# Kernel optimization log

Hardware: AMD Instinct MI355X
Metric: run time of the kernel (lower is better)

## Reference

```python
import jax, jax.numpy as jnp
import numpy as np

B, C, Ci, V = 1024, 256, 128, 90
EPS = 1e-5


def setup_inputs() -> dict:
    key = jax.random.key(0)
    ks = iter(jax.random.split(key, 40))
    def nrm(shape, s=1.0):
        return jax.random.normal(next(ks), shape, jnp.float32) * s
    def uni(shape):
        return jax.random.uniform(next(ks), shape, jnp.float32, 0.5, 1.5)
    inp = {"x1": nrm((B, C, V)), "x2": nrm((B, C, V))}
    for p in ["g", "th", "ph"]:
        inp[p + "_bn_gamma"] = uni((C,))
        inp[p + "_bn_beta"] = nrm((C,), 0.1)
        inp[p + "_bn_mean"] = nrm((C,), 0.1)
        inp[p + "_bn_var"] = uni((C,))
        inp[p + "_w"] = nrm((Ci, C), 0.05)
        inp[p + "_b"] = nrm((Ci,), 0.05)
    inp["W_w"] = nrm((C, Ci), 0.05)
    inp["W_b"] = nrm((C,), 0.05)
    inp["W_bn_gamma"] = uni((C,))
    inp["W_bn_beta"] = nrm((C,), 0.1)
    inp["W_bn_mean"] = nrm((C,), 0.1)
    inp["W_bn_var"] = uni((C,))
    inp["qt_w"] = nrm((Ci, C), 0.05); inp["qt_b"] = nrm((Ci,), 0.05)
    inp["ks_w"] = nrm((Ci, V), 0.05); inp["ks_b"] = nrm((Ci,), 0.05)
    inp["qs_w"] = nrm((Ci, V), 0.05); inp["qs_b"] = nrm((Ci,), 0.05)
    inp["kt_w"] = nrm((Ci, C), 0.05); inp["kt_b"] = nrm((Ci,), 0.05)
    return inp


def _bn(x, g, b, m, v):
    # eval-mode BatchNorm1d over channel dim of (B, C, V)
    return (x - m[:, None]) * jax.lax.rsqrt(v[:, None] + EPS) * g[:, None] + b[:, None]


def _conv1(x, w, b):
    # 1x1 Conv1d: (B, Cin, V) x (Cout, Cin) -> (B, Cout, V)
    return jnp.einsum('bcv,oc->bov', x, w) + b[:, None]


def reference(x1, x2,
              g_bn_gamma, g_bn_beta, g_bn_mean, g_bn_var, g_w, g_b,
              th_bn_gamma, th_bn_beta, th_bn_mean, th_bn_var, th_w, th_b,
              ph_bn_gamma, ph_bn_beta, ph_bn_mean, ph_bn_var, ph_w, ph_b,
              W_w, W_b, W_bn_gamma, W_bn_beta, W_bn_mean, W_bn_var,
              qt_w, qt_b, ks_w, ks_b, qs_w, qs_b, kt_w, kt_b):
    g_x1 = _conv1(_bn(x1, g_bn_gamma, g_bn_beta, g_bn_mean, g_bn_var), g_w, g_b)
    g_x2 = _conv1(_bn(x2, g_bn_gamma, g_bn_beta, g_bn_mean, g_bn_var), g_w, g_b)
    theta = _conv1(_bn(x1, th_bn_gamma, th_bn_beta, th_bn_mean, th_bn_var), th_w, th_b)  # theta(x1)
    phi = _conv1(_bn(x2, ph_bn_gamma, ph_bn_beta, ph_bn_mean, ph_bn_var), ph_w, ph_b)    # phi(x2)

    e_time = jnp.einsum('biv,bjv->bij', theta, phi)   # (B, Ci, Ci) = theta_x1 @ phi_x2
    e_space = jnp.einsum('bci,bcj->bij', theta, phi)  # (B, V, V)  = theta_x2 @ phi_x1

    attn_time_1 = jax.nn.softmax(e_time, axis=-1)
    attn_time_2 = jax.nn.softmax(jnp.swapaxes(e_time, 1, 2), axis=-1)
    attn_space_2 = jax.nn.softmax(e_space, axis=-1)
    attn_space_1 = jax.nn.softmax(jnp.swapaxes(e_space, 1, 2), axis=-1)

    z1 = jnp.einsum('bij,bjv,bvw->biw', attn_time_2, g_x1, attn_space_2)  # (B, Ci, V)
    z2 = jnp.einsum('bij,bjv,bvw->biw', attn_time_1, g_x2, attn_space_1)

    m1t = x1.mean(axis=2)                      # (B, C)
    q_time = m1t @ qt_w.T + qt_b               # (B, Ci)
    k_space = x2.mean(axis=1) @ ks_w.T + ks_b  # (B, Ci)
    # bmm of (B,1,Ci) x (B,Ci,1) -> (B,1,1); softmax over singleton dim == 1 (kept for faithfulness)
    attn_t2s = jax.nn.softmax(jnp.sum(q_time * k_space, axis=-1, keepdims=True)[:, :, None], axis=-1)
    x2n = x2 + attn_t2s * m1t[:, :, None]      # broadcast (B,1,1)*(B,C,1) over V

    q_space = x1.mean(axis=1) @ qs_w.T + qs_b  # (B, Ci)
    k_time = x2n.mean(axis=2) @ kt_w.T + kt_b  # (B, Ci)
    attn_s2t = jax.nn.softmax(jnp.sum(q_space * k_time, axis=-1, keepdims=True)[:, :, None], axis=-1)
    x1n = x1 + attn_s2t * x2n.mean(axis=1)[:, None, :]

    def Wop(z):
        return _bn(_conv1(z, W_w, W_b), W_bn_gamma, W_bn_beta, W_bn_mean, W_bn_var)

    return (x1n + Wop(z1), x2n + Wop(z2))
```

## Files before the change

### kernel.cpp

```cpp
#include <hip/hip_runtime.h>

namespace {

constexpr int B = 1024;

using u16 = unsigned short;
using u32 = unsigned int;

typedef __attribute__((ext_vector_type(8))) short bf16x8;
typedef __attribute__((ext_vector_type(4))) float f32x4;

#define MFMA16(a, b, c) __builtin_amdgcn_mfma_f32_16x16x32_bf16(a, b, c, 0, 0, 0)

__device__ __forceinline__ u16 f2bf(float f) {
  u32 u = __builtin_bit_cast(u32, f);
  u += 0x7FFFu + ((u >> 16) & 1u);
  return (u16)(u >> 16);
}
__device__ __forceinline__ float bf2f(u16 s) {
  u32 u = ((u32)s) << 16;
  return __builtin_bit_cast(float, u);
}
__device__ __forceinline__ u32 packbf2(float a, float b) {
  return (u32)f2bf(a) | ((u32)f2bf(b) << 16);
}

__global__ __launch_bounds__(256) void k0_fold(
    const float* __restrict__ gg, const float* __restrict__ gbe, const float* __restrict__ gme, const float* __restrict__ gva,
    const float* __restrict__ gw, const float* __restrict__ gbi,
    const float* __restrict__ tg, const float* __restrict__ tbe, const float* __restrict__ tme, const float* __restrict__ tva,
    const float* __restrict__ tw, const float* __restrict__ tbi,
    const float* __restrict__ pg, const float* __restrict__ pbe, const float* __restrict__ pme, const float* __restrict__ pva,
    const float* __restrict__ pw, const float* __restrict__ pbi,
    const float* __restrict__ Ww, const float* __restrict__ Wb,
    const float* __restrict__ Wg2, const float* __restrict__ Wbe, const float* __restrict__ Wme, const float* __restrict__ Wva,
    u16* __restrict__ wgo, float* __restrict__ bgo,
    u16* __restrict__ wthi, u16* __restrict__ wtlo, float* __restrict__ bto,
    u16* __restrict__ wphi, u16* __restrict__ wplo, float* __restrict__ bpo,
    u16* __restrict__ wWo, float* __restrict__ bWo)
{
  __shared__ float red[4];
  const int blk = blockIdx.x, tid = threadIdx.x;
  if (blk < 384) {
    const int p = blk >> 7, o = blk & 127;
    const float *ga, *be, *me, *va, *wm, *bi;
    if (p == 0)      { ga = gg; be = gbe; me = gme; va = gva; wm = gw; bi = gbi; }
    else if (p == 1) { ga = tg; be = tbe; me = tme; va = tva; wm = tw; bi = tbi; }
    else             { ga = pg; be = pbe; me = pme; va = pva; wm = pw; bi = pbi; }
    float s = ga[tid] * rsqrtf(va[tid] + 1e-5f);
    float t = be[tid] - me[tid] * s;
    float wv = wm[o * 256 + tid];
    float val = wv * s;
    if (p == 0) {
      wgo[o * 256 + tid] = f2bf(val);
    } else {
      u16 hi = f2bf(val);
      u16 lo = f2bf(val - bf2f(hi));
      if (p == 1) { wthi[o * 256 + tid] = hi; wtlo[o * 256 + tid] = lo; }
      else        { wphi[o * 256 + tid] = hi; wplo[o * 256 + tid] = lo; }
    }
    float part = t * wv;
#pragma unroll
    for (int off = 32; off; off >>= 1) part += __shfl_down(part, off);
    if ((tid & 63) == 0) red[tid >> 6] = part;
    __syncthreads();
    if (tid == 0) {
      float bsum = bi[o] + red[0] + red[1] + red[2] + red[3];
      if (p == 0) bgo[o] = bsum; else if (p == 1) bto[o] = bsum; else bpo[o] = bsum;
    }
  } else {
    const int c = blk - 384;
    float sW = Wg2[c] * rsqrtf(Wva[c] + 1e-5f);
    if (tid < 128) wWo[c * 128 + tid] = f2bf(Ww[c * 128 + tid] * sW);
    if (tid == 0) bWo[c] = Wb[c] * sW + Wbe[c] - Wme[c] * sW;
  }
}

__global__ __launch_bounds__(512, 4) void k1_conv(
    const float* __restrict__ x1, const float* __restrict__ x2,
    const u16* __restrict__ wG, const float* __restrict__ bG,
    const u16* __restrict__ wTh, const u16* __restrict__ wTl, const float* __restrict__ bT,
    const u16* __restrict__ wPh, const u16* __restrict__ wPl, const float* __restrict__ bP,
    u32* __restrict__ thRm, u32* __restrict__ phRm,
    u16* __restrict__ outU,
    float* __restrict__ m1t, float* __restrict__ x2cm, float* __restrict__ x1am)
{
  __shared__ u32 qb[64 * 92];
  __shared__ u16 xh[96 * 136];
  __shared__ u16 xl[96 * 136];
  __shared__ float red[4];
  const int b = blockIdx.x, tid = threadIdx.x;
  const int l = tid & 63, wv = tid >> 6, lr = l & 15, lq = l >> 4;
  const f32x4 zero = {0.f, 0.f, 0.f, 0.f};

  auto doPhase = [&](const float* __restrict__ xb,
                     const u16* __restrict__ Wh, const u16* __restrict__ Wl, const float* __restrict__ biasT,
                     u32* __restrict__ rmDst, u32* __restrict__ pkDst, u16* __restrict__ gDst, bool isX1) {
    f32x4 aT[6], aG[6];
#pragma unroll
    for (int i = 0; i < 6; ++i) { aT[i] = zero; aG[i] = zero; }
    float cs = 0.f;
    for (int h = 0; h < 2; ++h) {
      for (int q = 0; q < 2; ++q) {
        __syncthreads();
        const float* src = xb + (2 * h + q) * 5760;
        for (int t = tid; t < 2880; t += 512) {
          float2 f = *(const float2*)(src + 2 * t);
          int cl = (2 * t) / 90, v = 2 * t - 90 * cl;
          u16 h0 = f2bf(f.x); u16 l0 = f2bf(f.x - bf2f(h0));
          u16 h1 = f2bf(f.y); u16 l1 = f2bf(f.y - bf2f(h1));
          uint2 w; w.x = (u32)h0 | ((u32)l0 << 16); w.y = (u32)h1 | ((u32)l1 << 16);
          *(uint2*)&qb[cl * 92 + v] = w;
        }
        __syncthreads();
        for (int t = tid; t < 1440; t += 512) {
          int v = t % 90, c4 = t / 90;
          u32 p0 = qb[(4 * c4 + 0) * 92 + v], p1 = qb[(4 * c4 + 1) * 92 + v];
          u32 p2 = qb[(4 * c4 + 2) * 92 + v], p3 = qb[(4 * c4 + 3) * 92 + v];
          uint2 hi, lo;
          hi.x = (p0 & 0xFFFFu) | (p1 << 16);
          hi.y = (p2 & 0xFFFFu) | (p3 << 16);
          lo.x = (p0 >> 16) | (p1 & 0xFFFF0000u);
          lo.y = (p2 >> 16) | (p3 & 0xFFFF0000u);
          int base = v * 136 + 64 * q + 4 * c4;
          *(uint2*)&xh[base] = hi;
          *(uint2*)&xl[base] = lo;
        }
        if (q == 1) {
          for (int t = tid; t < 384; t += 512) {
            int v = 90 + (t >> 6), c2 = (t & 63) * 2;
            *(u32*)&xh[v * 136 + c2] = 0u;
            *(u32*)&xl[v * 136 + c2] = 0u;
          }
        }
      }
      __syncthreads();
      if (isX1) {
        if (tid < 128) {
          float s = 0.f;
          for (int v = 0; v < 90; ++v) s += bf2f(xh[v * 136 + tid]) + bf2f(xl[v * 136 + tid]);
          m1t[b * 256 + 128 * h + tid] = s * (1.f / 90.f);
#pragma unroll
          for (int o = 32; o; o >>= 1) s += __shfl_down(s, o);
          if ((tid & 63) == 0) red[(tid >> 6) + 2 * h] = s;
        }
      } else {
        if (tid < 90) {
          float s = 0.f;
          for (int cl = 0; cl < 128; ++cl) s += bf2f(xh[tid * 136 + cl]) + bf2f(xl[tid * 136 + cl]);
          cs += s;
        }
      }
      for (int kk = 0; kk < 4; ++kk) {
        const int wo = (16 * wv + lr) * 256 + 128 * h + kk * 32 + 8 * lq;
        bf16x8 ah = *(const bf16x8*)(Wh + wo);
        bf16x8 al = *(const bf16x8*)(Wl + wo);
        bf16x8 ag = *(const bf16x8*)(wG + wo);
#pragma unroll
        for (int nt = 0; nt < 6; ++nt) {
          const int bo = (16 * nt + lr) * 136 + kk * 32 + 8 * lq;
          bf16x8 bh = *(const bf16x8*)&xh[bo];
          bf16x8 bl = *(const bf16x8*)&xl[bo];
          aT[nt] = MFMA16(ah, bh, aT[nt]);
          aT[nt] = MFMA16(ah, bl, aT[nt]);
          aT[nt] = MFMA16(al, bh, aT[nt]);
          aG[nt] = MFMA16(ag, bh, aG[nt]);
        }
      }
    }
    __syncthreads();
    const int c0 = 16 * wv + 4 * lq;
    const float4 bt4 = *(const float4*)(biasT + c0);
    const float4 bg4 = *(const float4*)(bG + c0);
#pragma unroll
    for (int nt = 0; nt < 6; ++nt) {
      const int v = 16 * nt + lr;
      u32 pk0, pk1, pk2, pk3; uint2 gpk;
      if (v < 90) {
        float t0 = aT[nt][0] + bt4.x, t1 = aT[nt][1] + bt4.y;
        float t2 = aT[nt][2] + bt4.z, t3 = aT[nt][3] + bt4.w;
        u16 h0 = f2bf(t0), h1 = f2bf(t1), h2 = f2bf(t2), h3 = f2bf(t3);
        pk0 = (u32)h0 | ((u32)f2bf(t0 - bf2f(h0)) << 16);
        pk1 = (u32)h1 | ((u32)f2bf(t1 - bf2f(h1)) << 16);
        pk2 = (u32)h2 | ((u32)f2bf(t2 - bf2f(h2)) << 16);
        pk3 = (u32)h3 | ((u32)f2bf(t3 - bf2f(h3)) << 16);
        gpk.x = packbf2(aG[nt][0] + bg4.x, aG[nt][1] + bg4.y);
        gpk.y = packbf2(aG[nt][2] + bg4.z, aG[nt][3] + bg4.w);
      } else { pk0 = pk1 = pk2 = pk3 = 0u; gpk.x = 0u; gpk.y = 0u; }
      uint4 q4; q4.x = pk0; q4.y = pk1; q4.z = pk2; q4.w = pk3;
      *(uint4*)(pkDst + v * 128 + c0) = q4;
      rmDst[(c0 + 0) * 96 + v] = pk0;
      rmDst[(c0 + 1) * 96 + v] = pk1;
      rmDst[(c0 + 2) * 96 + v] = pk2;
      rmDst[(c0 + 3) * 96 + v] = pk3;
      *(uint2*)(gDst + v * 128 + c0) = gpk;
    }
    if (isX1) {
      if (tid == 0) x1am[b] = (red[0] + red[1] + red[2] + red[3]) * (1.f / 23040.f);
    } else {
      if (tid < 90) x2cm[b * 96 + tid] = cs * (1.f / 256.f);
    }
  };

  u16* o1 = outU + (size_t)b * 46080;
  u16* o2 = outU + (size_t)(1024 + b) * 46080;
  doPhase(x1 + (size_t)b * 23040, wTh, wTl, bT,
          thRm + (size_t)b * 12288, (u32*)(o1 + 12288), o1, true);
  doPhase(x2 + (size_t)b * 23040, wPh, wPl, bP,
          phRm + (size_t)b * 12288, (u32*)(o2 + 12288), o2, false);
}

__global__ __launch_bounds__(512) void k2_attn(
    const u32* __restrict__ thRm, const u32* __restrict__ phRm,
    u16* __restrict__ outU,
    u16* __restrict__ At1g, u16* __restrict__ At2g)
{
  __shared__ __align__(16) char smem[108544];
  u16* s0 = (u16*)smem;
  float* st = (float*)(smem + 106496);
  float* eL = (float*)smem;

  const int b = blockIdx.x, tid = threadIdx.x;
  const int l = tid & 63, wv = tid >> 6, lr = l & 15, lq = l >> 4;
  const f32x4 zero = {0.f, 0.f, 0.f, 0.f};

  const u32* thRmB = thRm + (size_t)b * 12288;
  const u32* phRmB = phRm + (size_t)b * 12288;
  const u32* thPk = (const u32*)(outU + (size_t)b * 46080 + 12288);
  const u32* phPk = (const u32*)(outU + (size_t)(1024 + b) * 46080 + 12288);
  u32* S1 = (u32*)(outU + (size_t)(1024 + b) * 46080 + 36864);
  u32* S2 = (u32*)(outU + (size_t)b * 46080 + 36864);

  u16* th_hi = s0;
  u16* th_lo = s0 + 13312;
  u16* ph_hi = s0 + 26624;
  u16* ph_lo = s0 + 39936;
  for (int d = tid; d < 6144; d += 512) {
    int ten = (d >= 3072);
    int i = d - 3072 * ten;
    int ci = i / 24, q4 = i - 24 * ci;
    uint4 P = *(const uint4*)((ten ? phRmB : thRmB) + ci * 96 + 4 * q4);
    uint2 hi, lo;
    hi.x = (P.x & 0xFFFFu) | (P.y << 16);
    hi.y = (P.z & 0xFFFFu) | (P.w << 16);
    lo.x = (P.x >> 16) | (P.y & 0xFFFF0000u);
    lo.y = (P.z >> 16) | (P.w & 0xFFFF0000u);
    *(uint2*)((ten ? ph_hi : th_hi) + ci * 104 + 4 * q4) = hi;
    *(uint2*)((ten ? ph_lo : th_lo) + ci * 104 + 4 * q4) = lo;
  }
  __syncthreads();
  f32x4 acc[8];
#pragma unroll
  for (int nt = 0; nt < 8; ++nt) acc[nt] = zero;
#pragma unroll
  for (int kk = 0; kk < 3; ++kk) {
    const int ao = (16 * wv + lr) * 104 + kk * 32 + 8 * lq;
    bf16x8 ah = *(const bf16x8*)&th_hi[ao];
    bf16x8 al = *(const bf16x8*)&th_lo[ao];
#pragma unroll
    for (int nt = 0; nt < 8; ++nt) {
      const int bo = (16 * nt + lr) * 104 + kk * 32 + 8 * lq;
      bf16x8 bh = *(const bf16x8*)&ph_hi[bo];
      bf16x8 bl = *(const bf16x8*)&ph_lo[bo];
      acc[nt] = MFMA16(ah, bh, acc[nt]);
      acc[nt] = MFMA16(ah, bl, acc[nt]);
      acc[nt] = MFMA16(al, bh, acc[nt]);
    }
  }
  __syncthreads();
#pragma unroll
  for (int nt = 0; nt < 8; ++nt)
#pragma unroll
    for (int r = 0; r < 4; ++r)
      eL[(16 * nt + lr) * 133 + 16 * wv + 4 * lq + r] = acc[nt][r];
  __syncthreads();
  if (tid < 128) {
    int j = tid; float m = -1e30f;
    for (int i = 0; i < 128; ++i) m = fmaxf(m, eL[j * 133 + i]);
    float s = 0.f;
    for (int i = 0; i < 128; ++i) s += __expf(eL[j * 133 + i] - m);
    st[j] = m; st[128 + j] = 1.f / s;
  } else if (tid < 256) {
    int i = tid - 128; float m = -1e30f;
    for (int j = 0; j < 128; ++j) m = fmaxf(m, eL[j * 133 + i]);
    float s = 0.f;
    for (int j = 0; j < 128; ++j) s += __expf(eL[j * 133 + i] - m);
    st[256 + i] = m; st[384 + i] = 1.f / s;
  }
  __syncthreads();
  {
    u32* A1 = (u32*)(At1g + (size_t)b * 16384);
    u32* A2 = (u32*)(At2g + (size_t)b * 16384);
    for (int d = tid; d < 8192; d += 512) {
      int i = d >> 6, jp = d & 63;
      float m1 = st[256 + i], s1v = st[384 + i];
      float a0 = __expf(eL[(2 * jp) * 133 + i] - m1) * s1v;
      float a1 = __expf(eL[(2 * jp + 1) * 133 + i] - m1) * s1v;
      A1[d] = packbf2(a0, a1);
      float m2 = st[i], s2v = st[128 + i];
      float b0 = __expf(eL[i * 133 + 2 * jp] - m2) * s2v;
      float b1 = __expf(eL[i * 133 + 2 * jp + 1] - m2) * s2v;
      A2[d] = packbf2(b0, b1);
    }
  }
  __syncthreads();

  u16* tTh = s0;
  u16* tTl = s0 + 13056;
  u16* pTh = s0 + 26112;
  u16* pTl = s0 + 39168;
  for (int d = tid; d < 6144; d += 512) {
    int ten = (d >= 3072);
    int i = d - 3072 * ten;
    int v = i >> 5, q4 = i & 31;
    uint4 P = *(const uint4*)((ten ? phPk : thPk) + v * 128 + 4 * q4);
    uint2 hi, lo;
    hi.x = (P.x & 0xFFFFu) | (P.y << 16);
    hi.y = (P.z & 0xFFFFu) | (P.w << 16);
    lo.x = (P.x >> 16) | (P.y & 0xFFFF0000u);
    lo.y = (P.z >> 16) | (P.w & 0xFFFF0000u);
    *(uint2*)((ten ? pTh : tTh) + v * 136 + 4 * q4) = hi;
    *(uint2*)((ten ? pTl : tTl) + v * 136 + 4 * q4) = lo;
  }
  __syncthreads();
  f32x4 accS[5];
#pragma unroll
  for (int it = 0; it < 5; ++it) accS[it] = zero;
#pragma unroll
  for (int it = 0; it < 5; ++it) {
    const int t5 = wv + 8 * it;
    if (t5 < 36) {
      const int mt = t5 / 6, nt = t5 - 6 * (t5 / 6);
#pragma unroll
      for (int kk = 0; kk < 4; ++kk) {
        const int ao = (16 * mt + lr) * 136 + kk * 32 + 8 * lq;
        const int bo = (16 * nt + lr) * 136 + kk * 32 + 8 * lq;
        bf16x8 ah = *(const bf16x8*)&tTh[ao];
        bf16x8 al = *(const bf16x8*)&tTl[ao];
        bf16x8 bh = *(const bf16x8*)&pTh[bo];
        bf16x8 bl = *(const bf16x8*)&pTl[bo];
        accS[it] = MFMA16(ah, bh, accS[it]);
        accS[it] = MFMA16(ah, bl, accS[it]);
        accS[it] = MFMA16(al, bh, accS[it]);
      }
    }
  }
  __syncthreads();
  {
    float* esL = (float*)smem;
#pragma unroll
    for (int it = 0; it < 5; ++it) {
      const int t5 = wv + 8 * it;
      if (t5 < 36) {
        const int mt = t5 / 6, nt = t5 - 6 * (t5 / 6);
#pragma unroll
        for (int r = 0; r < 4; ++r)
          esL[(16 * nt + lr) * 101 + 16 * mt + 4 * lq + r] = accS[it][r];
      }
    }
  }
  __syncthreads();
  {
    float* esL = (float*)smem;
    if (tid < 96) {
      int v = tid; float m = -1e30f;
      for (int w2 = 0; w2 < 90; ++w2) m = fmaxf(m, esL[v * 101 + w2]);
      float s = 0.f;
      for (int w2 = 0; w2 < 90; ++w2) s += __expf(esL[v * 101 + w2] - m);
      st[v] = m; st[128 + v] = 1.f / s;
    } else if (tid >= 128 && tid < 224) {
      int v = tid - 128; float m = -1e30f;
      for (int w2 = 0; w2 < 90; ++w2) m = fmaxf(m, esL[w2 * 101 + v]);
      float s = 0.f;
      for (int w2 = 0; w2 < 90; ++w2) s += __expf(esL[w2 * 101 + v] - m);
      st[256 + v] = m; st[384 + v] = 1.f / s;
    }
  }
  __syncthreads();
  {
    float* esL = (float*)smem;
    for (int d = tid; d < 4608; d += 512) {
      int w2 = d / 48, vp = d - 48 * (d / 48);
      int v0 = 2 * vp, v1 = v0 + 1;
      float a0 = __expf(esL[v0 * 101 + w2] - st[v0]) * st[128 + v0];
      float a1 = __expf(esL[v1 * 101 + w2] - st[v1]) * st[128 + v1];
      S1[d] = packbf2(a0, a1);
      float b0 = __expf(esL[w2 * 101 + v0] - st[256 + v0]) * st[384 + v0];
      float b1 = __expf(esL[w2 * 101 + v1] - st[256 + v1]) * st[384 + v1];
      S2[d] = packbf2(b0, b1);
    }
  }
}

__global__ __launch_bounds__(256) void k3_out(
    const float* __restrict__ x1, const float* __restrict__ x2,
    const u16* __restrict__ At1g, const u16* __restrict__ At2g,
    const u16* __restrict__ wW, const float* __restrict__ bW,
    const float* __restrict__ m1t, const float* __restrict__ x2cm, const float* __restrict__ x1am,
    float* __restrict__ out)
{
  __shared__ u16 gT[96 * 136];
  __shared__ u16 Tb[128 * 104];
  __shared__ u16 ZT[96 * 136];
  const int b = blockIdx.x, tid = threadIdx.x;
  const int l = tid & 63, wv = tid >> 6, lr = l & 15, lq = l >> 4;
  const f32x4 zero = {0.f, 0.f, 0.f, 0.f};

  float* out1 = out + (size_t)b * 23040;
  float* out2 = out + (size_t)23040 * 1024 + (size_t)b * 23040;
  const u16* g1s = (const u16*)out1;
  const u16* g2s = (const u16*)out2;
  const u16* As1 = (const u16*)out2 + 36864;
  const u16* As2 = (const u16*)out1 + 36864;

  auto phase = [&](const u16* __restrict__ gsrc, const u16* __restrict__ At,
                   const u16* __restrict__ AsT, const float* __restrict__ xres,
                   float* __restrict__ dst, bool modeA) {
    for (int i = tid; i < 1536; i += 256) {
      int v = i >> 4, hh = i & 15;
      *(uint4*)&gT[v * 136 + 8 * hh] = ((const uint4*)gsrc)[i];
    }
    __syncthreads();
#pragma unroll
    for (int ni = 0; ni < 2; ++ni) {
      const int nt = 2 * wv + ni;
      f32x4 acc[6];
#pragma unroll
      for (int i = 0; i < 6; ++i) acc[i] = zero;
#pragma unroll
      for (int kk = 0; kk < 4; ++kk) {
        bf16x8 bb = *(const bf16x8*)(At + (16 * nt + lr) * 128 + kk * 32 + 8 * lq);
#pragma unroll
        for (int mt = 0; mt < 6; ++mt) {
          bf16x8 a = *(const bf16x8*)&gT[(16 * mt + lr) * 136 + kk * 32 + 8 * lq];
          acc[mt] = MFMA16(a, bb, acc[mt]);
        }
      }
#pragma unroll
      for (int mt = 0; mt < 6; ++mt) {
        uint2 pk;
        pk.x = packbf2(acc[mt][0], acc[mt][1]);
        pk.y = packbf2(acc[mt][2], acc[mt][3]);
        *(uint2*)&Tb[(16 * nt + lr) * 104 + 16 * mt + 4 * lq] = pk;
      }
    }
    __syncthreads();
    {
      f32x4 acc[2][6];
#pragma unroll
      for (int i = 0; i < 2; ++i)
#pragma unroll
        for (int j = 0; j < 6; ++j) acc[i][j] = zero;
#pragma unroll
      for (int kk = 0; kk < 3; ++kk) {
        bf16x8 a0 = *(const bf16x8*)&Tb[(16 * (2 * wv) + lr) * 104 + kk * 32 + 8 * lq];
        bf16x8 a1 = *(const bf16x8*)&Tb[(16 * (2 * wv + 1) + lr) * 104 + kk * 32 + 8 * lq];
#pragma unroll
        for (int nt = 0; nt < 6; ++nt) {
          bf16x8 bb = *(const bf16x8*)(AsT + (16 * nt + lr) * 96 + kk * 32 + 8 * lq);
          acc[0][nt] = MFMA16(a0, bb, acc[0][nt]);
          acc[1][nt] = MFMA16(a1, bb, acc[1][nt]);
        }
      }
#pragma unroll
      for (int mi = 0; mi < 2; ++mi) {
        const int mt = 2 * wv + mi;
#pragma unroll
        for (int nt = 0; nt < 6; ++nt) {
          uint2 pk;
          pk.x = packbf2(acc[mi][nt][0], acc[mi][nt][1]);
          pk.y = packbf2(acc[mi][nt][2], acc[mi][nt][3]);
          *(uint2*)&ZT[(16 * nt + lr) * 136 + 16 * mt + 4 * lq] = pk;
        }
      }
    }
    __syncthreads();
    const float am = modeA ? 0.f : x1am[b];
#pragma unroll
    for (int mi = 0; mi < 4; ++mi) {
      const int mt = 4 * wv + mi;
      f32x4 acc[6];
#pragma unroll
      for (int i = 0; i < 6; ++i) acc[i] = zero;
#pragma unroll
      for (int kk = 0; kk < 4; ++kk) {
        bf16x8 a = *(const bf16x8*)(wW + (16 * mt + lr) * 128 + kk * 32 + 8 * lq);
#pragma unroll
        for (int nt = 0; nt < 6; ++nt) {
          bf16x8 bb = *(const bf16x8*)&ZT[(16 * nt + lr) * 136 + kk * 32 + 8 * lq];
          acc[nt] = MFMA16(a, bb, acc[nt]);
        }
      }
      const int c0 = 16 * mt + 4 * lq;
      const float4 bw4 = *(const float4*)(bW + c0);
      float bwA[4] = {bw4.x, bw4.y, bw4.z, bw4.w};
      float mA[4] = {0.f, 0.f, 0.f, 0.f};
      if (modeA) {
        const float4 m4 = *(const float4*)(m1t + b * 256 + c0);
        mA[0] = m4.x; mA[1] = m4.y; mA[2] = m4.z; mA[3] = m4.w;
      }
#pragma unroll
      for (int nt = 0; nt < 6; ++nt) {
        const int v = 16 * nt + lr;
        if (v < 90) {
          const float addv = modeA ? 0.f : (am + x2cm[b * 96 + v]);
#pragma unroll
          for (int r = 0; r < 4; ++r) {
            const int c = c0 + r;
            const float extra = modeA ? mA[r] : addv;
            dst[c * 90 + v] = xres[c * 90 + v] + acc[nt][r] + bwA[r] + extra;
          }
        }
      }
    }
    __syncthreads();
  };

  phase(g2s, At1g + (size_t)b * 16384, As1, x2 + (size_t)b * 23040, out2, true);
  phase(g1s, At2g + (size_t)b * 16384, As2, x1 + (size_t)b * 23040, out1, false);
}

}

extern "C" void kernel_launch(void* const* d_in, const int* in_sizes, int n_in,
                              void* d_out, int out_size, void* d_ws, size_t ws_size,
                              hipStream_t stream)
{
  (void)in_sizes; (void)n_in; (void)out_size; (void)ws_size;
  const float* x1  = (const float*)d_in[0];
  const float* x2  = (const float*)d_in[1];
  const float* gg  = (const float*)d_in[2];
  const float* gbe = (const float*)d_in[3];
  const float* gme = (const float*)d_in[4];
  const float* gva = (const float*)d_in[5];
  const float* gw  = (const float*)d_in[6];
  const float* gbi = (const float*)d_in[7];
  const float* tg  = (const float*)d_in[8];
  const float* tbe = (const float*)d_in[9];
  const float* tme = (const float*)d_in[10];
  const float* tva = (const float*)d_in[11];
  const float* tw  = (const float*)d_in[12];
  const float* tbi = (const float*)d_in[13];
  const float* pg  = (const float*)d_in[14];
  const float* pbe = (const float*)d_in[15];
  const float* pme = (const float*)d_in[16];
  const float* pva = (const float*)d_in[17];
  const float* pw  = (const float*)d_in[18];
  const float* pbi = (const float*)d_in[19];
  const float* Ww  = (const float*)d_in[20];
  const float* Wb  = (const float*)d_in[21];
  const float* Wg  = (const float*)d_in[22];
  const float* Wbe = (const float*)d_in[23];
  const float* Wme = (const float*)d_in[24];
  const float* Wva = (const float*)d_in[25];

  float* out = (float*)d_out;
  unsigned char* W8 = (unsigned char*)d_ws;

  size_t off = 0;
  auto al = [&](size_t n) { size_t r = off; off += (n + 255) & ~(size_t)255; return r; };
  const size_t oWG  = al(65536);
  const size_t oWTh = al(65536), oWTl = al(65536);
  const size_t oWPh = al(65536), oWPl = al(65536);
  const size_t oWW  = al(65536);
  const size_t oBG = al(512), oBT = al(512), oBP = al(512), oBW = al(1024);
  const size_t oRM1 = al((size_t)B * 49152), oRM2 = al((size_t)B * 49152);
  const size_t oA1 = al((size_t)B * 32768), oA2 = al((size_t)B * 32768);
  const size_t oM1 = al((size_t)B * 1024), oXC = al((size_t)B * 384), oXA = al((size_t)B * 4);

  k0_fold<<<dim3(640), dim3(256), 0, stream>>>(
      gg, gbe, gme, gva, gw, gbi,
      tg, tbe, tme, tva, tw, tbi,
      pg, pbe, pme, pva, pw, pbi,
      Ww, Wb, Wg, Wbe, Wme, Wva,
      (u16*)(W8 + oWG), (float*)(W8 + oBG),
      (u16*)(W8 + oWTh), (u16*)(W8 + oWTl), (float*)(W8 + oBT),
      (u16*)(W8 + oWPh), (u16*)(W8 + oWPl), (float*)(W8 + oBP),
      (u16*)(W8 + oWW), (float*)(W8 + oBW));

  k1_conv<<<dim3(B), dim3(512), 0, stream>>>(
      x1, x2,
      (const u16*)(W8 + oWG), (const float*)(W8 + oBG),
      (const u16*)(W8 + oWTh), (const u16*)(W8 + oWTl), (const float*)(W8 + oBT),
      (const u16*)(W8 + oWPh), (const u16*)(W8 + oWPl), (const float*)(W8 + oBP),
      (u32*)(W8 + oRM1), (u32*)(W8 + oRM2),
      (u16*)out,
      (float*)(W8 + oM1), (float*)(W8 + oXC), (float*)(W8 + oXA));

  k2_attn<<<dim3(B), dim3(512), 0, stream>>>(
      (const u32*)(W8 + oRM1), (const u32*)(W8 + oRM2),
      (u16*)out,
      (u16*)(W8 + oA1), (u16*)(W8 + oA2));

  k3_out<<<dim3(B), dim3(256), 0, stream>>>(
      x1, x2,
      (const u16*)(W8 + oA1), (const u16*)(W8 + oA2),
      (const u16*)(W8 + oWW), (const float*)(W8 + oBW),
      (const float*)(W8 + oM1), (const float*)(W8 + oXC), (const float*)(W8 + oXA),
      out);
}
```

Measured before the change: 450.5 us.

## Split per-batch phases across two blocks in conv, attention and output kernels

Each of the three main kernels now launches two blocks per batch element instead of one, with each block handling one of the formerly sequential phases (x1 vs x2 conv, time-attention vs space-attention, out1 vs out2). The goal is to double grid parallelism and shorten per-block critical paths on a 1024-block grid. The column-sum for x2 is moved to read the staging buffer, and a cheaper truncating hi/lo split (tsplit) replaces the rounding split. The g conv also gains an extra MFMA using the low part, which adds compute. Truncation changes the rounding of the hi half, but the lo half still captures the residual.

```diff
diff --git a/kernel.cpp b/kernel.cpp
--- a/kernel.cpp
+++ b/kernel.cpp
@@ -23,6 +23,12 @@
 }
 __device__ __forceinline__ u32 packbf2(float a, float b) {
   return (u32)f2bf(a) | ((u32)f2bf(b) << 16);
+}
+__device__ __forceinline__ u32 tsplit(float f) {
+  u32 u = __builtin_bit_cast(u32, f);
+  float r = f - __builtin_bit_cast(float, u & 0xFFFF0000u);
+  u32 ur = __builtin_bit_cast(u32, r);
+  return (u >> 16) | (ur & 0xFFFF0000u);
 }
 
 __global__ __launch_bounds__(256) void k0_fold(
@@ -89,125 +95,121 @@
   __shared__ u16 xh[96 * 136];
   __shared__ u16 xl[96 * 136];
   __shared__ float red[4];
-  const int b = blockIdx.x, tid = threadIdx.x;
+  const int bid = blockIdx.x, tid = threadIdx.x;
+  const int b = bid >> 1; const bool isX1 = !(bid & 1);
   const int l = tid & 63, wv = tid >> 6, lr = l & 15, lq = l >> 4;
   const f32x4 zero = {0.f, 0.f, 0.f, 0.f};
 
-  auto doPhase = [&](const float* __restrict__ xb,
-                     const u16* __restrict__ Wh, const u16* __restrict__ Wl, const float* __restrict__ biasT,
-                     u32* __restrict__ rmDst, u32* __restrict__ pkDst, u16* __restrict__ gDst, bool isX1) {
-    f32x4 aT[6], aG[6];
-#pragma unroll
-    for (int i = 0; i < 6; ++i) { aT[i] = zero; aG[i] = zero; }
-    float cs = 0.f;
-    for (int h = 0; h < 2; ++h) {
-      for (int q = 0; q < 2; ++q) {
-        __syncthreads();
-        const float* src = xb + (2 * h + q) * 5760;
-        for (int t = tid; t < 2880; t += 512) {
-          float2 f = *(const float2*)(src + 2 * t);
-          int cl = (2 * t) / 90, v = 2 * t - 90 * cl;
-          u16 h0 = f2bf(f.x); u16 l0 = f2bf(f.x - bf2f(h0));
-          u16 h1 = f2bf(f.y); u16 l1 = f2bf(f.y - bf2f(h1));
-          uint2 w; w.x = (u32)h0 | ((u32)l0 << 16); w.y = (u32)h1 | ((u32)l1 << 16);
-          *(uint2*)&qb[cl * 92 + v] = w;
+  const float* xb = (isX1 ? x1 : x2) + (size_t)b * 23040;
+  const u16* Wh = isX1 ? wTh : wPh;
+  const u16* Wl = isX1 ? wTl : wPl;
+  const float* biasT = isX1 ? bT : bP;
+  u16* oSl = outU + (size_t)(isX1 ? b : 1024 + b) * 46080;
+  u32* rmDst = (isX1 ? thRm : phRm) + (size_t)b * 12288;
+  u32* pkDst = (u32*)(oSl + 12288);
+  u16* gDst = oSl;
+
+  f32x4 aT[6], aG[6];
+#pragma unroll
+  for (int i = 0; i < 6; ++i) { aT[i] = zero; aG[i] = zero; }
+  float cs = 0.f;
+
+  for (int h = 0; h < 2; ++h) {
+    for (int q = 0; q < 2; ++q) {
+      __syncthreads();
+      const float* src = xb + (2 * h + q) * 5760;
+      for (int t = tid; t < 2880; t += 512) {
+        float2 f = *(const float2*)(src + 2 * t);
+        int cl = (2 * t) / 90, v = 2 * t - 90 * cl;
+        uint2 w; w.x = tsplit(f.x); w.y = tsplit(f.y);
+        *(uint2*)&qb[cl * 92 + v] = w;
+      }
+      __syncthreads();
+      for (int t = tid; t < 1440; t += 512) {
+        int v = t % 90, c4 = t / 90;
+        u32 p0 = qb[(4 * c4 + 0) * 92 + v], p1 = qb[(4 * c4 + 1) * 92 + v];
+        u32 p2 = qb[(4 * c4 + 2) * 92 + v], p3 = qb[(4 * c4 + 3) * 92 + v];
+        uint2 hi, lo;
+        hi.x = (p0 & 0xFFFFu) | (p1 << 16);
+        hi.y = (p2 & 0xFFFFu) | (p3 << 16);
+        lo.x = (p0 >> 16) | (p1 & 0xFFFF0000u);
+        lo.y = (p2 >> 16) | (p3 & 0xFFFF0000u);
+        int base = v * 136 + 64 * q + 4 * c4;
+        *(uint2*)&xh[base] = hi;
+        *(uint2*)&xl[base] = lo;
+      }
+      if (q == 1) {
+        for (int t = tid; t < 384; t += 512) {
+          int v = 90 + (t >> 6), c2 = (t & 63) * 2;
+          *(u32*)&xh[v * 136 + c2] = 0u;
+          *(u32*)&xl[v * 136 + c2] = 0u;
         }
-        __syncthreads();
-        for (int t = tid; t < 1440; t += 512) {
-          int v = t % 90, c4 = t / 90;
-          u32 p0 = qb[(4 * c4 + 0) * 92 + v], p1 = qb[(4 * c4 + 1) * 92 + v];
-          u32 p2 = qb[(4 * c4 + 2) * 92 + v], p3 = qb[(4 * c4 + 3) * 92 + v];
-          uint2 hi, lo;
-          hi.x = (p0 & 0xFFFFu) | (p1 << 16);
-          hi.y = (p2 & 0xFFFFu) | (p3 << 16);
-          lo.x = (p0 >> 16) | (p1 & 0xFFFF0000u);
-          lo.y = (p2 >> 16) | (p3 & 0xFFFF0000u);
-          int base = v * 136 + 64 * q + 4 * c4;
-          *(uint2*)&xh[base] = hi;
-          *(uint2*)&xl[base] = lo;
+      }
+      if (!isX1 && tid < 90) {
+        float s = 0.f;
+        for (int cl = 0; cl < 64; ++cl) {
+          u32 p = qb[cl * 92 + tid];
+          s += bf2f((u16)p) + bf2f((u16)(p >> 16));
         }
-        if (q == 1) {
-          for (int t = tid; t < 384; t += 512) {
-            int v = 90 + (t >> 6), c2 = (t & 63) * 2;
-            *(u32*)&xh[v * 136 + c2] = 0u;
-            *(u32*)&xl[v * 136 + c2] = 0u;
-          }
-        }
-      }
-      __syncthreads();
-      if (isX1) {
-        if (tid < 128) {
-          float s = 0.f;
-          for (int v = 0; v < 90; ++v) s += bf2f(xh[v * 136 + tid]) + bf2f(xl[v * 136 + tid]);
-          m1t[b * 256 + 128 * h + tid] = s * (1.f / 90.f);
-#pragma unroll
-          for (int o = 32; o; o >>= 1) s += __shfl_down(s, o);
-          if ((tid & 63) == 0) red[(tid >> 6) + 2 * h] = s;
-        }
-      } else {
-        if (tid < 90) {
-          float s = 0.f;
-          for (int cl = 0; cl < 128; ++cl) s += bf2f(xh[tid * 136 + cl]) + bf2f(xl[tid * 136 + cl]);
-          cs += s;
-        }
-      }
-      for (int kk = 0; kk < 4; ++kk) {
-        const int wo = (16 * wv + lr) * 256 + 128 * h + kk * 32 + 8 * lq;
-        bf16x8 ah = *(const bf16x8*)(Wh + wo);
-        bf16x8 al = *(const bf16x8*)(Wl + wo);
-        bf16x8 ag = *(const bf16x8*)(wG + wo);
-#pragma unroll
-        for (int nt = 0; nt < 6; ++nt) {
-          const int bo = (16 * nt + lr) * 136 + kk * 32 + 8 * lq;
-          bf16x8 bh = *(const bf16x8*)&xh[bo];
-          bf16x8 bl = *(const bf16x8*)&xl[bo];
-          aT[nt] = MFMA16(ah, bh, aT[nt]);
-          aT[nt] = MFMA16(ah, bl, aT[nt]);
-          aT[nt] = MFMA16(al, bh, aT[nt]);
-          aG[nt] = MFMA16(ag, bh, aG[nt]);
-        }
+        cs += s;
       }
     }
     __syncthreads();
-    const int c0 = 16 * wv + 4 * lq;
-    const float4 bt4 = *(const float4*)(biasT + c0);
-    const float4 bg4 = *(const float4*)(bG + c0);
-#pragma unroll
-    for (int nt = 0; nt < 6; ++nt) {
-      const int v = 16 * nt + lr;
-      u32 pk0, pk1, pk2, pk3; uint2 gpk;
-      if (v < 90) {
-        float t0 = aT[nt][0] + bt4.x, t1 = aT[nt][1] + bt4.y;
-        float t2 = aT[nt][2] + bt4.z, t3 = aT[nt][3] + bt4.w;
-        u16 h0 = f2bf(t0), h1 = f2bf(t1), h2 = f2bf(t2), h3 = f2bf(t3);
-        pk0 = (u32)h0 | ((u32)f2bf(t0 - bf2f(h0)) << 16);
-        pk1 = (u32)h1 | ((u32)f2bf(t1 - bf2f(h1)) << 16);
-        pk2 = (u32)h2 | ((u32)f2bf(t2 - bf2f(h2)) << 16);
-        pk3 = (u32)h3 | ((u32)f2bf(t3 - bf2f(h3)) << 16);
-        gpk.x = packbf2(aG[nt][0] + bg4.x, aG[nt][1] + bg4.y);
-        gpk.y = packbf2(aG[nt][2] + bg4.z, aG[nt][3] + bg4.w);
-      } else { pk0 = pk1 = pk2 = pk3 = 0u; gpk.x = 0u; gpk.y = 0u; }
-      uint4 q4; q4.x = pk0; q4.y = pk1; q4.z = pk2; q4.w = pk3;
-      *(uint4*)(pkDst + v * 128 + c0) = q4;
-      rmDst[(c0 + 0) * 96 + v] = pk0;
-      rmDst[(c0 + 1) * 96 + v] = pk1;
-      rmDst[(c0 + 2) * 96 + v] = pk2;
-      rmDst[(c0 + 3) * 96 + v] = pk3;
-      *(uint2*)(gDst + v * 128 + c0) = gpk;
-    }
-    if (isX1) {
-      if (tid == 0) x1am[b] = (red[0] + red[1] + red[2] + red[3]) * (1.f / 23040.f);
-    } else {
-      if (tid < 90) x2cm[b * 96 + tid] = cs * (1.f / 256.f);
-    }
-  };
-
-  u16* o1 = outU + (size_t)b * 46080;
-  u16* o2 = outU + (size_t)(1024 + b) * 46080;
-  doPhase(x1 + (size_t)b * 23040, wTh, wTl, bT,
-          thRm + (size_t)b * 12288, (u32*)(o1 + 12288), o1, true);
-  doPhase(x2 + (size_t)b * 23040, wPh, wPl, bP,
-          phRm + (size_t)b * 12288, (u32*)(o2 + 12288), o2, false);
+    if (isX1 && tid < 128) {
+      float s = 0.f;
+      for (int v = 0; v < 90; ++v) s += bf2f(xh[v * 136 + tid]) + bf2f(xl[v * 136 + tid]);
+      m1t[b * 256 + 128 * h + tid] = s * (1.f / 90.f);
+#pragma unroll
+      for (int o = 32; o; o >>= 1) s += __shfl_down(s, o);
+      if ((tid & 63) == 0) red[(tid >> 6) + 2 * h] = s;
+    }
+    for (int kk = 0; kk < 4; ++kk) {
+      const int wo = (16 * wv + lr) * 256 + 128 * h + kk * 32 + 8 * lq;
+      bf16x8 ah = *(const bf16x8*)(Wh + wo);
+      bf16x8 al = *(const bf16x8*)(Wl + wo);
+      bf16x8 ag = *(const bf16x8*)(wG + wo);
+#pragma unroll
+      for (int nt = 0; nt < 6; ++nt) {
+        const int bo = (16 * nt + lr) * 136 + kk * 32 + 8 * lq;
+        bf16x8 bh = *(const bf16x8*)&xh[bo];
+        bf16x8 bl = *(const bf16x8*)&xl[bo];
+        aT[nt] = MFMA16(ah, bh, aT[nt]);
+        aT[nt] = MFMA16(ah, bl, aT[nt]);
+        aT[nt] = MFMA16(al, bh, aT[nt]);
+        aG[nt] = MFMA16(ag, bh, aG[nt]);
+        aG[nt] = MFMA16(ag, bl, aG[nt]);
+      }
+    }
+  }
+  __syncthreads();
+  const int c0 = 16 * wv + 4 * lq;
+  const float4 bt4 = *(const float4*)(biasT + c0);
+  const float4 bg4 = *(const float4*)(bG + c0);
+#pragma unroll
+  for (int nt = 0; nt < 6; ++nt) {
+    const int v = 16 * nt + lr;
+    u32 pk0, pk1, pk2, pk3; uint2 gpk;
+    if (v < 90) {
+      pk0 = tsplit(aT[nt][0] + bt4.x);
+      pk1 = tsplit(aT[nt][1] + bt4.y);
+      pk2 = tsplit(aT[nt][2] + bt4.z);
+      pk3 = tsplit(aT[nt][3] + bt4.w);
+      gpk.x = packbf2(aG[nt][0] + bg4.x, aG[nt][1] + bg4.y);
+      gpk.y = packbf2(aG[nt][2] + bg4.z, aG[nt][3] + bg4.w);
+    } else { pk0 = pk1 = pk2 = pk3 = 0u; gpk.x = 0u; gpk.y = 0u; }
+    uint4 q4; q4.x = pk0; q4.y = pk1; q4.z = pk2; q4.w = pk3;
+    *(uint4*)(pkDst + v * 128 + c0) = q4;
+    rmDst[(c0 + 0) * 96 + v] = pk0;
+    rmDst[(c0 + 1) * 96 + v] = pk1;
+    rmDst[(c0 + 2) * 96 + v] = pk2;
+    rmDst[(c0 + 3) * 96 + v] = pk3;
+    *(uint2*)(gDst + v * 128 + c0) = gpk;
+  }
+  if (isX1) {
+    if (tid == 0) x1am[b] = (red[0] + red[1] + red[2] + red[3]) * (1.f / 23040.f);
+  } else {
+    if (tid < 90) x2cm[b * 96 + tid] = cs * (1.f / 256.f);
+  }
 }
 
 __global__ __launch_bounds__(512) void k2_attn(
@@ -220,75 +222,71 @@
   float* st = (float*)(smem + 106496);
   float* eL = (float*)smem;
 
-  const int b = blockIdx.x, tid = threadIdx.x;
+  const int bid = blockIdx.x, tid = threadIdx.x;
+  const int b = bid >> 1;
   const int l = tid & 63, wv = tid >> 6, lr = l & 15, lq = l >> 4;
   const f32x4 zero = {0.f, 0.f, 0.f, 0.f};
 
-  const u32* thRmB = thRm + (size_t)b * 12288;
-  const u32* phRmB = phRm + (size_t)b * 12288;
-  const u32* thPk = (const u32*)(outU + (size_t)b * 46080 + 12288);
-  const u32* phPk = (const u32*)(outU + (size_t)(1024 + b) * 46080 + 12288);
-  u32* S1 = (u32*)(outU + (size_t)(1024 + b) * 46080 + 36864);
-  u32* S2 = (u32*)(outU + (size_t)b * 46080 + 36864);
-
-  u16* th_hi = s0;
-  u16* th_lo = s0 + 13312;
-  u16* ph_hi = s0 + 26624;
-  u16* ph_lo = s0 + 39936;
-  for (int d = tid; d < 6144; d += 512) {
-    int ten = (d >= 3072);
-    int i = d - 3072 * ten;
-    int ci = i / 24, q4 = i - 24 * ci;
-    uint4 P = *(const uint4*)((ten ? phRmB : thRmB) + ci * 96 + 4 * q4);
-    uint2 hi, lo;
-    hi.x = (P.x & 0xFFFFu) | (P.y << 16);
-    hi.y = (P.z & 0xFFFFu) | (P.w << 16);
-    lo.x = (P.x >> 16) | (P.y & 0xFFFF0000u);
-    lo.y = (P.z >> 16) | (P.w & 0xFFFF0000u);
-    *(uint2*)((ten ? ph_hi : th_hi) + ci * 104 + 4 * q4) = hi;
-    *(uint2*)((ten ? ph_lo : th_lo) + ci * 104 + 4 * q4) = lo;
-  }
-  __syncthreads();
-  f32x4 acc[8];
-#pragma unroll
-  for (int nt = 0; nt < 8; ++nt) acc[nt] = zero;
-#pragma unroll
-  for (int kk = 0; kk < 3; ++kk) {
-    const int ao = (16 * wv + lr) * 104 + kk * 32 + 8 * lq;
-    bf16x8 ah = *(const bf16x8*)&th_hi[ao];
-    bf16x8 al = *(const bf16x8*)&th_lo[ao];
-#pragma unroll
-    for (int nt = 0; nt < 8; ++nt) {
-      const int bo = (16 * nt + lr) * 104 + kk * 32 + 8 * lq;
-      bf16x8 bh = *(const bf16x8*)&ph_hi[bo];
-      bf16x8 bl = *(const bf16x8*)&ph_lo[bo];
-      acc[nt] = MFMA16(ah, bh, acc[nt]);
-      acc[nt] = MFMA16(ah, bl, acc[nt]);
-      acc[nt] = MFMA16(al, bh, acc[nt]);
-    }
-  }
-  __syncthreads();
-#pragma unroll
-  for (int nt = 0; nt < 8; ++nt)
-#pragma unroll
-    for (int r = 0; r < 4; ++r)
-      eL[(16 * nt + lr) * 133 + 16 * wv + 4 * lq + r] = acc[nt][r];
-  __syncthreads();
-  if (tid < 128) {
-    int j = tid; float m = -1e30f;
-    for (int i = 0; i < 128; ++i) m = fmaxf(m, eL[j * 133 + i]);
-    float s = 0.f;
-    for (int i = 0; i < 128; ++i) s += __expf(eL[j * 133 + i] - m);
-    st[j] = m; st[128 + j] = 1.f / s;
-  } else if (tid < 256) {
-    int i = tid - 128; float m = -1e30f;
-    for (int j = 0; j < 128; ++j) m = fmaxf(m, eL[j * 133 + i]);
-    float s = 0.f;
-    for (int j = 0; j < 128; ++j) s += __expf(eL[j * 133 + i] - m);
-    st[256 + i] = m; st[384 + i] = 1.f / s;
-  }
-  __syncthreads();
-  {
+  if (!(bid & 1)) {
+    const u32* thRmB = thRm + (size_t)b * 12288;
+    const u32* phRmB = phRm + (size_t)b * 12288;
+    u16* th_hi = s0;
+    u16* th_lo = s0 + 13312;
+    u16* ph_hi = s0 + 26624;
+    u16* ph_lo = s0 + 39936;
+    for (int d = tid; d < 6144; d += 512) {
+      int ten = (d >= 3072);
+      int i = d - 3072 * ten;
+      int ci = i / 24, q4 = i - 24 * ci;
+      uint4 P = *(const uint4*)((ten ? phRmB : thRmB) + ci * 96 + 4 * q4);
+      uint2 hi, lo;
+      hi.x = (P.x & 0xFFFFu) | (P.y << 16);
+      hi.y = (P.z & 0xFFFFu) | (P.w << 16);
+      lo.x = (P.x >> 16) | (P.y & 0xFFFF0000u);
+      lo.y = (P.z >> 16) | (P.w & 0xFFFF0000u);
+      *(uint2*)((ten ? ph_hi : th_hi) + ci * 104 + 4 * q4) = hi;
+      *(uint2*)((ten ? ph_lo : th_lo) + ci * 104 + 4 * q4) = lo;
+    }
+    __syncthreads();
+    f32x4 acc[8];
+#pragma unroll
+    for (int nt = 0; nt < 8; ++nt) acc[nt] = zero;
+#pragma unroll
+    for (int kk = 0; kk < 3; ++kk) {
+      const int ao = (16 * wv + lr) * 104 + kk * 32 + 8 * lq;
+      bf16x8 ah = *(const bf16x8*)&th_hi[ao];
+      bf16x8 al = *(const bf16x8*)&th_lo[ao];
+#pragma unroll
+      for (int nt = 0; nt < 8; ++nt) {
+        const int bo = (16 * nt + lr) * 104 + kk * 32 + 8 * lq;
+        bf16x8 bh = *(const bf16x8*)&ph_hi[bo];
+        bf16x8 bl = *(const bf16x8*)&ph_lo[bo];
+        acc[nt] = MFMA16(ah, bh, acc[nt]);
+        acc[nt] = MFMA16(ah, bl, acc[nt]);
+        acc[nt] = MFMA16(al, bh, acc[nt]);
+      }
+    }
+    __syncthreads();
+#pragma unroll
+    for (int nt = 0; nt < 8; ++nt)
+#pragma unroll
+      for (int r = 0; r < 4; ++r)
+        eL[(16 * nt + lr) * 133 + 16 * wv + 4 * lq + r] = acc[nt][r];
+    __syncthreads();
+    if (tid < 128) {
+      int j = tid; float m = -1e30f;
+      for (int i = 0; i < 128; ++i) m = fmaxf(m, eL[j * 133 + i]);
+      float s = 0.f;
+      for (int i = 0; i < 128; ++i) s += __expf(eL[j * 133 + i] - m);
+      st[j] = m; st[128 + j] = 1.f / s;
+    } else if (tid < 256) {
+      int i = tid - 128; float m = -1e30f;
+      for (int j = 0; j < 128; ++j) m = fmaxf(m, eL[j * 133 + i]);
+      float s = 0.f;
+      for (int j = 0; j < 128; ++j) s += __expf(eL[j * 133 + i] - m);
+      st[256 + i] = m; st[384 + i] = 1.f / s;
+    }
+    __syncthreads();
     u32* A1 = (u32*)(At1g + (size_t)b * 16384);
     u32* A2 = (u32*)(At2g + (size_t)b * 16384);
     for (int d = tid; d < 8192; d += 512) {
@@ -302,8 +300,13 @@
       float b1 = __expf(eL[i * 133 + 2 * jp + 1] - m2) * s2v;
       A2[d] = packbf2(b0, b1);
     }
-  }
-  __syncthreads();
+    return;
+  }
+
+  const u32* thPk = (const u32*)(outU + (size_t)b * 46080 + 12288);
+  const u32* phPk = (const u32*)(outU + (size_t)(1024 + b) * 46080 + 12288);
+  u32* S1 = (u32*)(outU + (size_t)(1024 + b) * 46080 + 36864);
+  u32* S2 = (u32*)(outU + (size_t)b * 46080 + 36864);
 
   u16* tTh = s0;
   u16* tTl = s0 + 13056;
@@ -402,122 +405,120 @@
   __shared__ u16 gT[96 * 136];
   __shared__ u16 Tb[128 * 104];
   __shared__ u16 ZT[96 * 136];
-  const int b = blockIdx.x, tid = threadIdx.x;
+  const int bid = blockIdx.x, tid = threadIdx.x;
+  const int b = bid >> 1; const bool modeA = !(bid & 1);
   const int l = tid & 63, wv = tid >> 6, lr = l & 15, lq = l >> 4;
   const f32x4 zero = {0.f, 0.f, 0.f, 0.f};
 
   float* out1 = out + (size_t)b * 23040;
   float* out2 = out + (size_t)23040 * 1024 + (size_t)b * 23040;
-  const u16* g1s = (const u16*)out1;
-  const u16* g2s = (const u16*)out2;
-  const u16* As1 = (const u16*)out2 + 36864;
-  const u16* As2 = (const u16*)out1 + 36864;
-
-  auto phase = [&](const u16* __restrict__ gsrc, const u16* __restrict__ At,
-                   const u16* __restrict__ AsT, const float* __restrict__ xres,
-                   float* __restrict__ dst, bool modeA) {
-    for (int i = tid; i < 1536; i += 256) {
-      int v = i >> 4, hh = i & 15;
-      *(uint4*)&gT[v * 136 + 8 * hh] = ((const uint4*)gsrc)[i];
-    }
-    __syncthreads();
-#pragma unroll
-    for (int ni = 0; ni < 2; ++ni) {
-      const int nt = 2 * wv + ni;
-      f32x4 acc[6];
-#pragma unroll
-      for (int i = 0; i < 6; ++i) acc[i] = zero;
-#pragma unroll
-      for (int kk = 0; kk < 4; ++kk) {
-        bf16x8 bb = *(const bf16x8*)(At + (16 * nt + lr) * 128 + kk * 32 + 8 * lq);
-#pragma unroll
-        for (int mt = 0; mt < 6; ++mt) {
-          bf16x8 a = *(const bf16x8*)&gT[(16 * mt + lr) * 136 + kk * 32 + 8 * lq];
-          acc[mt] = MFMA16(a, bb, acc[mt]);
+
+  const u16* gsrc; const u16* At; const u16* AsT; const float* xres; float* dst;
+  if (modeA) {
+    gsrc = (const u16*)out2; At = At1g + (size_t)b * 16384;
+    AsT = (const u16*)out2 + 36864; xres = x2 + (size_t)b * 23040; dst = out2;
+  } else {
+    gsrc = (const u16*)out1; At = At2g + (size_t)b * 16384;
+    AsT = (const u16*)out1 + 36864; xres = x1 + (size_t)b * 23040; dst = out1;
+  }
+
+  for (int i = tid; i < 1536; i += 256) {
+    int v = i >> 4, hh = i & 15;
+    *(uint4*)&gT[v * 136 + 8 * hh] = ((const uint4*)gsrc)[i];
+  }
+  __syncthreads();
+#pragma unroll
+  for (int ni = 0; ni < 2; ++ni) {
+    const int nt = 2 * wv + ni;
+    f32x4 acc[6];
+#pragma unroll
+    for (int i = 0; i < 6; ++i) acc[i] = zero;
+#pragma unroll
+    for (int kk = 0; kk < 4; ++kk) {
+      bf16x8 bb = *(const bf16x8*)(At + (16 * nt + lr) * 128 + kk * 32 + 8 * lq);
+#pragma unroll
+      for (int mt = 0; mt < 6; ++mt) {
+        bf16x8 a = *(const bf16x8*)&gT[(16 * mt + lr) * 136 + kk * 32 + 8 * lq];
+        acc[mt] = MFMA16(a, bb, acc[mt]);
+      }
+    }
+#pragma unroll
+    for (int mt = 0; mt < 6; ++mt) {
+      uint2 pk;
+      pk.x = packbf2(acc[mt][0], acc[mt][1]);
+      pk.y = packbf2(acc[mt][2], acc[mt][3]);
+      *(uint2*)&Tb[(16 * nt + lr) * 104 + 16 * mt + 4 * lq] = pk;
+    }
+  }
+  __syncthreads();
+  {
+    f32x4 acc[2][6];
+#pragma unroll
+    for (int i = 0; i < 2; ++i)
+#pragma unroll
+      for (int j = 0; j < 6; ++j) acc[i][j] = zero;
+#pragma unroll
+    for (int kk = 0; kk < 3; ++kk) {
+      bf16x8 a0 = *(const bf16x8*)&Tb[(16 * (2 * wv) + lr) * 104 + kk * 32 + 8 * lq];
+      bf16x8 a1 = *(const bf16x8*)&Tb[(16 * (2 * wv + 1) + lr) * 104 + kk * 32 + 8 * lq];
+#pragma unroll
+      for (int nt = 0; nt < 6; ++nt) {
+        bf16x8 bb = *(const bf16x8*)(AsT + (16 * nt + lr) * 96 + kk * 32 + 8 * lq);
+        acc[0][nt] = MFMA16(a0, bb, acc[0][nt]);
+        acc[1][nt] = MFMA16(a1, bb, acc[1][nt]);
+      }
+    }
+#pragma unroll
+    for (int mi = 0; mi < 2; ++mi) {
+      const int mt = 2 * wv + mi;
+#pragma unroll
+      for (int nt = 0; nt < 6; ++nt) {
+        uint2 pk;
+        pk.x = packbf2(acc[mi][nt][0], acc[mi][nt][1]);
+        pk.y = packbf2(acc[mi][nt][2], acc[mi][nt][3]);
+        *(uint2*)&ZT[(16 * nt + lr) * 136 + 16 * mt + 4 * lq] = pk;
+      }
+    }
+  }
+  __syncthreads();
+  const float am = modeA ? 0.f : x1am[b];
+#pragma unroll
+  for (int mi = 0; mi < 4; ++mi) {
+    const int mt = 4 * wv + mi;
+    f32x4 acc[6];
+#pragma unroll
+    for (int i = 0; i < 6; ++i) acc[i] = zero;
+#pragma unroll
+    for (int kk = 0; kk < 4; ++kk) {
+      bf16x8 a = *(const bf16x8*)(wW + (16 * mt + lr) * 128 + kk * 32 + 8 * lq);
+#pragma unroll
+      for (int nt = 0; nt < 6; ++nt) {
+        bf16x8 bb = *(const bf16x8*)&ZT[(16 * nt + lr) * 136 + kk * 32 + 8 * lq];
+        acc[nt] = MFMA16(a, bb, acc[nt]);
+      }
+    }
+    const int c0 = 16 * mt + 4 * lq;
+    const float4 bw4 = *(const float4*)(bW + c0);
+    float bwA[4] = {bw4.x, bw4.y, bw4.z, bw4.w};
+    float mA[4] = {0.f, 0.f, 0.f, 0.f};
+    if (modeA) {
+      const float4 m4 = *(const float4*)(m1t + b * 256 + c0);
+      mA[0] = m4.x; mA[1] = m4.y; mA[2] = m4.z; mA[3] = m4.w;
+    }
+#pragma unroll
+    for (int nt = 0; nt < 6; ++nt) {
+      const int v = 16 * nt + lr;
+      if (v < 90) {
+        const float addv = modeA ? 0.f : (am + x2cm[b * 96 + v]);
+#pragma unroll
+        for (int r = 0; r < 4; ++r) {
+          const int c = c0 + r;
+          const float extra = modeA ? mA[r] : addv;
+          dst[c * 90 + v] = xres[c * 90 + v] + acc[nt][r] + bwA[r] + extra;
         }
       }
-#pragma unroll
-      for (int mt = 0; mt < 6; ++mt) {
-        uint2 pk;
-        pk.x = packbf2(acc[mt][0], acc[mt][1]);
-        pk.y = packbf2(acc[mt][2], acc[mt][3]);
-        *(uint2*)&Tb[(16 * nt + lr) * 104 + 16 * mt + 4 * lq] = pk;
-      }
-    }
-    __syncthreads();
-    {
-      f32x4 acc[2][6];
-#pragma unroll
-      for (int i = 0; i < 2; ++i)
-#pragma unroll
-        for (int j = 0; j < 6; ++j) acc[i][j] = zero;
-#pragma unroll
-      for (int kk = 0; kk < 3; ++kk) {
-        bf16x8 a0 = *(const bf16x8*)&Tb[(16 * (2 * wv) + lr) * 104 + kk * 32 + 8 * lq];
-        bf16x8 a1 = *(const bf16x8*)&Tb[(16 * (2 * wv + 1) + lr) * 104 + kk * 32 + 8 * lq];
-#pragma unroll
-        for (int nt = 0; nt < 6; ++nt) {
-          bf16x8 bb = *(const bf16x8*)(AsT + (16 * nt + lr) * 96 + kk * 32 + 8 * lq);
-          acc[0][nt] = MFMA16(a0, bb, acc[0][nt]);
-          acc[1][nt] = MFMA16(a1, bb, acc[1][nt]);
-        }
-      }
-#pragma unroll
-      for (int mi = 0; mi < 2; ++mi) {
-        const int mt = 2 * wv + mi;
-#pragma unroll
-        for (int nt = 0; nt < 6; ++nt) {
-          uint2 pk;
-          pk.x = packbf2(acc[mi][nt][0], acc[mi][nt][1]);
-          pk.y = packbf2(acc[mi][nt][2], acc[mi][nt][3]);
-          *(uint2*)&ZT[(16 * nt + lr) * 136 + 16 * mt + 4 * lq] = pk;
-        }
-      }
-    }
-    __syncthreads();
-    const float am = modeA ? 0.f : x1am[b];
-#pragma unroll
-    for (int mi = 0; mi < 4; ++mi) {
-      const int mt = 4 * wv + mi;
-      f32x4 acc[6];
-#pragma unroll
-      for (int i = 0; i < 6; ++i) acc[i] = zero;
-#pragma unroll
-      for (int kk = 0; kk < 4; ++kk) {
-        bf16x8 a = *(const bf16x8*)(wW + (16 * mt + lr) * 128 + kk * 32 + 8 * lq);
-#pragma unroll
-        for (int nt = 0; nt < 6; ++nt) {
-          bf16x8 bb = *(const bf16x8*)&ZT[(16 * nt + lr) * 136 + kk * 32 + 8 * lq];
-          acc[nt] = MFMA16(a, bb, acc[nt]);
-        }
-      }
-      const int c0 = 16 * mt + 4 * lq;
-      const float4 bw4 = *(const float4*)(bW + c0);
-      float bwA[4] = {bw4.x, bw4.y, bw4.z, bw4.w};
-      float mA[4] = {0.f, 0.f, 0.f, 0.f};
-      if (modeA) {
-        const float4 m4 = *(const float4*)(m1t + b * 256 + c0);
-        mA[0] = m4.x; mA[1] = m4.y; mA[2] = m4.z; mA[3] = m4.w;
-      }
-#pragma unroll
-      for (int nt = 0; nt < 6; ++nt) {
-        const int v = 16 * nt + lr;
-        if (v < 90) {
-          const float addv = modeA ? 0.f : (am + x2cm[b * 96 + v]);
-#pragma unroll
-          for (int r = 0; r < 4; ++r) {
-            const int c = c0 + r;
-            const float extra = modeA ? mA[r] : addv;
-            dst[c * 90 + v] = xres[c * 90 + v] + acc[nt][r] + bwA[r] + extra;
-          }
-        }
-      }
-    }
-    __syncthreads();
-  };
-
-  phase(g2s, At1g + (size_t)b * 16384, As1, x2 + (size_t)b * 23040, out2, true);
-  phase(g1s, At2g + (size_t)b * 16384, As2, x1 + (size_t)b * 23040, out1, false);
+    }
+  }
 }
 
 }
@@ -578,7 +579,7 @@
       (u16*)(W8 + oWPh), (u16*)(W8 + oWPl), (float*)(W8 + oBP),
       (u16*)(W8 + oWW), (float*)(W8 + oBW));
 
-  k1_conv<<<dim3(B), dim3(512), 0, stream>>>(
+  k1_conv<<<dim3(2 * B), dim3(512), 0, stream>>>(
       x1, x2,
       (const u16*)(W8 + oWG), (const float*)(W8 + oBG),
       (const u16*)(W8 + oWTh), (const u16*)(W8 + oWTl), (const float*)(W8 + oBT),
@@ -587,12 +588,12 @@
       (u16*)out,
       (float*)(W8 + oM1), (float*)(W8 + oXC), (float*)(W8 + oXA));
 
-  k2_attn<<<dim3(B), dim3(512), 0, stream>>>(
+  k2_attn<<<dim3(2 * B), dim3(512), 0, stream>>>(
       (const u32*)(W8 + oRM1), (const u32*)(W8 + oRM2),
       (u16*)out,
       (u16*)(W8 + oA1), (u16*)(W8 + oA2));
 
-  k3_out<<<dim3(B), dim3(256), 0, stream>>>(
+  k3_out<<<dim3(2 * B), dim3(256), 0, stream>>>(
       x1, x2,
       (const u16*)(W8 + oA1), (const u16*)(W8 + oA2),
       (const u16*)(W8 + oWW), (const float*)(W8 + oBW),
```

After: 521.7 us. 1.16x slower.
